# Kernel optimization log

Hardware: AMD Instinct MI355X
Metric: run time of the kernel (lower is better)

The kernel has to match this reference:

```python
import jax, jax.numpy as jnp
import numpy as np

BETA = 1.0
GAMMA = 0.25


def setup_inputs() -> dict:
    key = jax.random.key(0)
    ks = jax.random.split(key, 8)
    N, D_in, D_h, D_z = 65536, 1024, 512, 256
    s = lambda fan_in: 1.0 / np.sqrt(fan_in)
    return {
        "x": jax.random.normal(ks[0], (N, D_in), jnp.float32),
        "eW1": jax.random.normal(ks[1], (D_in, D_h), jnp.float32) * s(D_in),
        "eb1": jnp.zeros((D_h,), jnp.float32),
        "eW2": jax.random.normal(ks[2], (D_h, D_z), jnp.float32) * s(D_h),
        "eb2": jnp.zeros((D_z,), jnp.float32),
        "dW1": jax.random.normal(ks[3], (D_z, D_h), jnp.float32) * s(D_z),
        "db1": jnp.zeros((D_h,), jnp.float32),
        "dW2": jax.random.normal(ks[4], (D_h, D_in), jnp.float32) * s(D_h),
        "db2": jnp.zeros((D_in,), jnp.float32),
        "C0": jax.random.normal(ks[5], (1024, D_z), jnp.float32),
        "C1": jax.random.normal(ks[6], (512, D_z), jnp.float32),
        "C2": jax.random.normal(ks[7], (256, D_z), jnp.float32),
    }


def _nearest_idx(r, C):
    # argmin of squared euclidean distance == argmin of cdist(p=2)
    r = jax.lax.stop_gradient(r)
    d2 = jnp.sum(r * r, -1, keepdims=True) - 2.0 * (r @ C.T) + jnp.sum(C * C, -1)
    return jnp.argmin(d2, axis=-1)


def reference(x, eW1, eb1, eW2, eb2, dW1, db1, dW2, db2, C0, C1, C2):
    sg = jax.lax.stop_gradient
    # encoder: Linear -> GELU (exact) -> Linear
    z = jax.nn.gelu(x @ eW1 + eb1, approximate=False) @ eW2 + eb2
    residual = z
    output = jnp.zeros_like(z)
    losses = []
    for C in (C0, C1, C2):
        idx = _nearest_idx(residual, sg(C))
        q = C[idx]                                    # [N, 256] gather
        z2c = jnp.mean((residual - sg(q)) ** 2)       # commit input to code
        c2z = jnp.mean((sg(residual) - q) ** 2)       # move code to input
        losses.append(BETA * c2z + GAMMA * z2c)
        output = output + q
        residual = residual - q
    # straight-through: z + sg(zq) - sg(z)
    h = z + sg(output) - sg(z)
    out = jax.nn.gelu(h @ dW1 + db1, approximate=False) @ dW2 + db2
    recon_loss = jnp.mean((out - x) ** 2)
    return jnp.stack([recon_loss] + losses)  # [4]: recon, commit0, commit1, commit2
```

## Files before the change

### kernel.cpp

```cpp
#include <hip/hip_runtime.h>
#include <cstddef>


typedef __attribute__((ext_vector_type(8))) __bf16 bf16x8;
typedef __attribute__((ext_vector_type(4))) float f32x4;
typedef unsigned short u16;

__device__ __forceinline__ u16 f2bf(float f) {
    unsigned u = __float_as_uint(f);
    u += 0x7fffu + ((u >> 16) & 1u);
    return (u16)(u >> 16);
}
__device__ __forceinline__ float bf2f(u16 b) {
    return __uint_as_float((unsigned)b << 16);
}
__device__ __forceinline__ float gelu_exact(float v) {
    return 0.5f * v * (1.0f + erff(v * 0.7071067811865475f));
}
__device__ __forceinline__ void gload16(const void* g, void* l) {
    __builtin_amdgcn_global_load_lds(
        (const __attribute__((address_space(1))) void*)g,
        (__attribute__((address_space(3))) void*)l, 16, 0, 0);
}
__device__ __forceinline__ f32x4 mfma_bf16(bf16x8 a, bf16x8 b, f32x4 c) {
    return __builtin_amdgcn_mfma_f32_16x16x32_bf16(a, b, c, 0, 0, 0);
}

__global__ __launch_bounds__(256)
void prep_x(const float* __restrict__ x, u16* __restrict__ xbf)
{
    const size_t total = (size_t)65536 * 1024;
    const size_t step  = (size_t)gridDim.x * 256 * 8;
    for (size_t i = ((size_t)blockIdx.x * 256 + threadIdx.x) * 8; i < total; i += step) {
        float4 v0 = *(const float4*)&x[i];
        float4 v1 = *(const float4*)&x[i + 4];
        uint4 o;
        o.x = (unsigned)f2bf(v0.x) | ((unsigned)f2bf(v0.y) << 16);
        o.y = (unsigned)f2bf(v0.z) | ((unsigned)f2bf(v0.w) << 16);
        o.z = (unsigned)f2bf(v1.x) | ((unsigned)f2bf(v1.y) << 16);
        o.w = (unsigned)f2bf(v1.z) | ((unsigned)f2bf(v1.w) << 16);
        *(uint4*)&xbf[i] = o;
    }
}

__global__ __launch_bounds__(256)
void prep_weights(const float* __restrict__ eW1, const float* __restrict__ eW2,
                  const float* __restrict__ dW1, const float* __restrict__ dW2,
                  u16* __restrict__ eW1t, u16* __restrict__ eW2t,
                  u16* __restrict__ dW1t, u16* __restrict__ dW2t)
{
    const int b = blockIdx.x, t = threadIdx.x;
    if (b < 2048) {
        int e = b * 256 + t;
        int n = e >> 10, k = e & 1023;
        eW1t[e] = f2bf(eW1[(size_t)k * 512 + n]);
    } else if (b < 2560) {
        int e = (b - 2048) * 256 + t;
        int n = e >> 9, k = e & 511;
        eW2t[e] = f2bf(eW2[(size_t)k * 256 + n]);
    } else if (b < 3072) {
        int e = (b - 2560) * 256 + t;
        int n = e >> 8, k = e & 255;
        dW1t[e] = f2bf(dW1[(size_t)k * 512 + n]);
    } else {
        int e = (b - 3072) * 256 + t;
        int n = e >> 9, k = e & 511;
        dW2t[e] = f2bf(dW2[(size_t)k * 1024 + n]);
    }
}

__global__ __launch_bounds__(256)
void cb_prep(const float* __restrict__ C0, const float* __restrict__ C1,
             const float* __restrict__ C2, u16* __restrict__ Cbf,
             float* __restrict__ cnorm)
{
    __shared__ float red[256];
    const int code = blockIdx.x, t = threadIdx.x;
    const float* C;
    int local;
    if (code < 1024)      { C = C0; local = code; }
    else if (code < 1536) { C = C1; local = code - 1024; }
    else                  { C = C2; local = code - 1536; }
    const float v = C[(size_t)local * 256 + t];
    Cbf[(size_t)code * 256 + t] = f2bf(v);
    red[t] = v * v;
    __syncthreads();
    for (int s = 128; s; s >>= 1) { if (t < s) red[t] += red[t + s]; __syncthreads(); }
    if (t == 0) cnorm[code] = red[0];
}

template <int EPI>
__global__ __launch_bounds__(256, 2)
void gemm_mfma(const u16* __restrict__ A, const u16* __restrict__ Bt,
               const float* __restrict__ bias, u16* __restrict__ Obf,
               float* __restrict__ Of, const u16* __restrict__ Xbf,
               float* __restrict__ lossOut, int N, int K, int ntn,
               float lossScale)
{
    __shared__ __align__(16) u16 As[2][128 * 64];
    __shared__ __align__(16) u16 Bs[2][128 * 64];

    const int nwg = gridDim.x;
    const int bid = blockIdx.x;
    const int wg  = (bid & 7) * (nwg >> 3) + (bid >> 3);
    const int brow = (wg / ntn) * 128;
    const int bcol = (wg % ntn) * 128;

    const int t    = threadIdx.x;
    const int lane = t & 63;
    const int wid  = t >> 6;
    const int wrow = (wid >> 1) * 64, wcol = (wid & 1) * 64;
    const int lrow = lane & 15, g = lane >> 4;

    const int nt = K >> 6;

    f32x4 acc[4][4];
#pragma unroll
    for (int m = 0; m < 4; ++m)
#pragma unroll
        for (int n = 0; n < 4; ++n) acc[m][n] = (f32x4)0.f;

    auto stage = [&](const u16* __restrict__ src, int row0, int kt, u16* dst) {
#pragma unroll
        for (int it = 0; it < 4; ++it) {
            const int d   = (it * 256 + t) * 16;
            const int row = d >> 7;
            const int ch  = (d >> 4) & 7;
            const int cs  = ch ^ (row & 7);
            gload16(&src[(size_t)(row0 + row) * K + kt * 64 + cs * 8],
                    (char*)dst + d);
        }
    };

    stage(A, brow, 0, As[0]);
    stage(Bt, bcol, 0, Bs[0]);
    __syncthreads();

    int cur = 0;
    for (int kt = 0; kt < nt; ++kt) {
        if (kt + 1 < nt) {
            stage(A, brow, kt + 1, As[cur ^ 1]);
            stage(Bt, bcol, kt + 1, Bs[cur ^ 1]);
        }
#pragma unroll
        for (int ks = 0; ks < 2; ++ks) {
            bf16x8 a[4], b[4];
#pragma unroll
            for (int m = 0; m < 4; ++m) {
                const int R = wrow + m * 16 + lrow;
                a[m] = *(const bf16x8*)((const char*)&As[cur][0]
                         + R * 128 + (((ks * 4 + g) ^ (R & 7)) << 4));
            }
#pragma unroll
            for (int n = 0; n < 4; ++n) {
                const int R = wcol + n * 16 + lrow;
                b[n] = *(const bf16x8*)((const char*)&Bs[cur][0]
                         + R * 128 + (((ks * 4 + g) ^ (R & 7)) << 4));
            }
#pragma unroll
            for (int m = 0; m < 4; ++m)
#pragma unroll
                for (int n = 0; n < 4; ++n)
                    acc[m][n] = mfma_bf16(a[m], b[n], acc[m][n]);
        }
        __syncthreads();
        cur ^= 1;
    }

    int   colN[4];
    float bn[4];
#pragma unroll
    for (int n = 0; n < 4; ++n) {
        colN[n] = bcol + wcol + n * 16 + lrow;
        bn[n]   = bias[colN[n]];
    }

    if (EPI == 0) {
#pragma unroll
        for (int m = 0; m < 4; ++m) {
            const int rowb = brow + wrow + m * 16 + (lane >> 4) * 4;
#pragma unroll
            for (int n = 0; n < 4; ++n)
#pragma unroll
                for (int j = 0; j < 4; ++j)
                    Obf[(size_t)(rowb + j) * N + colN[n]] =
                        f2bf(gelu_exact(acc[m][n][j] + bn[n]));
        }
    } else if (EPI == 1) {
#pragma unroll
        for (int m = 0; m < 4; ++m) {
            const int rowb = brow + wrow + m * 16 + (lane >> 4) * 4;
#pragma unroll
            for (int n = 0; n < 4; ++n)
#pragma unroll
                for (int j = 0; j < 4; ++j)
                    Of[(size_t)(rowb + j) * N + colN[n]] = acc[m][n][j] + bn[n];
        }
    } else {
        float partial = 0.f;
#pragma unroll
        for (int m = 0; m < 4; ++m) {
            const int rowb = brow + wrow + m * 16 + (lane >> 4) * 4;
#pragma unroll
            for (int n = 0; n < 4; ++n)
#pragma unroll
                for (int j = 0; j < 4; ++j) {
                    const float o = acc[m][n][j] + bn[n];
                    const float d = o - bf2f(Xbf[(size_t)(rowb + j) * N + colN[n]]);
                    partial = fmaf(d, d, partial);
                }
        }
        float* red = (float*)&As[0][0];
        red[t] = partial;
        __syncthreads();
        for (int s = 128; s; s >>= 1) { if (t < s) red[t] += red[t + s]; __syncthreads(); }
        if (t == 0) atomicAdd(lossOut, red[0] * lossScale);
    }
}

__global__ __launch_bounds__(512, 4)
void vq_mfma(const float* __restrict__ Z, const u16* __restrict__ Cbf,
             const float* __restrict__ cnorm,
             const float* __restrict__ C0, const float* __restrict__ C1,
             const float* __restrict__ C2,
             u16* __restrict__ ZQ, float* __restrict__ lossOut)
{
    __shared__ __align__(16) u16 Rb[64][264];
    __shared__ __align__(16) u16 Cs[2][32 * 256];
    __shared__ float redv[64][2];
    __shared__ int   redi[64][2];
    __shared__ int   idxs[3][64];
    __shared__ float lred[8];

    const int t    = threadIdx.x;
    const int lane = t & 63;
    const int wid  = t >> 6;
    const int rg   = wid & 3;
    const int cg   = wid >> 2;
    const int lrow = lane & 15, g = lane >> 4;
    const int col  = t & 255;
    const int rh   = t >> 8;
    const int brow = blockIdx.x * 64;

    float R[32];
#pragma unroll
    for (int r = 0; r < 32; ++r)
        R[r] = Z[(size_t)(brow + rh * 32 + r) * 256 + col];

    const float* Cf[3]  = {C0, C1, C2};
    const int ncodes[3] = {1024, 512, 256};
    const int coff[3]   = {0, 1024, 1536};
    const float lscale  = 1.25f / (65536.0f * 256.0f);

    for (int stage = 0; stage < 3; ++stage) {
        const u16*   Cb  = Cbf + (size_t)coff[stage] * 256;
        const float* cns = cnorm + coff[stage];
        const int ntile  = ncodes[stage] >> 5;

        auto stageC = [&](int tile, int buf) {
#pragma unroll
            for (int it = 0; it < 2; ++it) {
                const int d   = (it * 512 + t) * 16;
                const int row = d >> 9;
                const int kb  = d & 511;
                const int kbs = kb ^ ((row & 7) << 4);
                gload16(&Cb[(size_t)(tile * 32 + row) * 256 + (kbs >> 1)],
                        (char*)&Cs[buf][0] + d);
            }
        };

        stageC(0, 0);
#pragma unroll
        for (int r = 0; r < 32; ++r) Rb[rh * 32 + r][col] = f2bf(R[r]);
        __syncthreads();

        bf16x8 a[8];
#pragma unroll
        for (int ks = 0; ks < 8; ++ks)
            a[ks] = *(const bf16x8*)&Rb[rg * 16 + lrow][ks * 32 + g * 8];

        float best[4]; int bidx[4];
#pragma unroll
        for (int j = 0; j < 4; ++j) { best[j] = 3.0e38f; bidx[j] = 0; }

        const int cr = cg * 16 + lrow;

        int buf = 0;
#pragma unroll 1
        for (int tile = 0; tile < ntile; ++tile) {
            if (tile + 1 < ntile) stageC(tile + 1, buf ^ 1);
            const int   code = tile * 32 + cr;
            const float cn   = cns[code];
            f32x4 acc = (f32x4)0.f;
#pragma unroll
            for (int ks = 0; ks < 8; ++ks) {
                const int kb = (ks * 64 + g * 16) ^ ((cr & 7) << 4);
                bf16x8 b = *(const bf16x8*)((const char*)&Cs[buf][0]
                             + cr * 512 + kb);
                acc = mfma_bf16(a[ks], b, acc);
            }
#pragma unroll
            for (int j = 0; j < 4; ++j) {
                const float s = fmaf(-2.0f, acc[j], cn);
                if (s < best[j]) { best[j] = s; bidx[j] = code; }
            }
            __syncthreads();
            buf ^= 1;
        }

#pragma unroll
        for (int j = 0; j < 4; ++j) {
            float v = best[j]; int i = bidx[j];
#pragma unroll
            for (int d = 1; d < 16; d <<= 1) {
                const float ov = __shfl_xor(v, d);
                const int   oi = __shfl_xor(i, d);
                if (ov < v || (ov == v && oi < i)) { v = ov; i = oi; }
            }
            if (lrow == 0) {
                redv[rg * 16 + g * 4 + j][cg] = v;
                redi[rg * 16 + g * 4 + j][cg] = i;
            }
        }
        __syncthreads();
        if (t < 64) {
            float v = redv[t][0]; int i = redi[t][0];
            const float ov = redv[t][1]; const int oi = redi[t][1];
            if (ov < v || (ov == v && oi < i)) { v = ov; i = oi; }
            idxs[stage][t] = i;
        }
        __syncthreads();

        const float* Cfs = Cf[stage];
        float partial = 0.f;
#pragma unroll
        for (int r = 0; r < 32; ++r) {
            const float q  = Cfs[(size_t)idxs[stage][rh * 32 + r] * 256 + col];
            const float rn = R[r] - q;
            R[r] = rn;
            partial = fmaf(rn, rn, partial);
        }
#pragma unroll
        for (int d = 32; d; d >>= 1) partial += __shfl_down(partial, d);
        if (lane == 0) lred[wid] = partial;
        __syncthreads();
        if (t == 0) {
            float s = 0.f;
#pragma unroll
            for (int w2 = 0; w2 < 8; ++w2) s += lred[w2];
            atomicAdd(&lossOut[1 + stage], s * lscale);
        }
        __syncthreads();
    }

#pragma unroll
    for (int r = 0; r < 32; ++r) {
        const int row = rh * 32 + r;
        const float zq = C0[(size_t)idxs[0][row] * 256 + col]
                       + C1[(size_t)idxs[1][row] * 256 + col]
                       + C2[(size_t)idxs[2][row] * 256 + col];
        ZQ[(size_t)(brow + row) * 256 + col] = f2bf(zq);
    }
}

extern "C" void kernel_launch(void* const* d_in, const int* in_sizes, int n_in,
                              void* d_out, int out_size, void* d_ws, size_t ws_size,
                              hipStream_t stream)
{
    const float* x   = (const float*)d_in[0];
    const float* eW1 = (const float*)d_in[1];
    const float* eb1 = (const float*)d_in[2];
    const float* eW2 = (const float*)d_in[3];
    const float* eb2 = (const float*)d_in[4];
    const float* dW1 = (const float*)d_in[5];
    const float* db1 = (const float*)d_in[6];
    const float* dW2 = (const float*)d_in[7];
    const float* db2 = (const float*)d_in[8];
    const float* C0  = (const float*)d_in[9];
    const float* C1  = (const float*)d_in[10];
    const float* C2  = (const float*)d_in[11];
    float* out = (float*)d_out;

    char* w = (char*)d_ws;
    u16*   H1   = (u16*)(w);
    float* Zf   = (float*)(w + ((size_t)64 << 20));
    u16*   ZQ   = (u16*)(w + ((size_t)128 << 20));
    u16*   H2   = (u16*)(w + ((size_t)160 << 20));
    u16*   xbf  = (u16*)(w + ((size_t)230 << 20));
    u16*   eW1t = (u16*)(w + ((size_t)224 << 20));
    u16*   eW2t = (u16*)(w + ((size_t)225 << 20));
    u16*   dW1t = (u16*)(w + ((size_t)226 << 20));
    u16*   dW2t = (u16*)(w + ((size_t)227 << 20));
    u16*   Cbf  = (u16*)(w + ((size_t)228 << 20));
    float* cn   = (float*)(w + ((size_t)229 << 20));

    hipMemsetAsync(d_out, 0, 4 * sizeof(float), stream);

    prep_x<<<4096, 256, 0, stream>>>(x, xbf);
    prep_weights<<<5120, 256, 0, stream>>>(eW1, eW2, dW1, dW2, eW1t, eW2t, dW1t, dW2t);
    cb_prep<<<1792, 256, 0, stream>>>(C0, C1, C2, Cbf, cn);

    gemm_mfma<0><<<2048, 256, 0, stream>>>(
        xbf, eW1t, eb1, H1, nullptr, nullptr, nullptr, 512, 1024, 4, 0.f);
    gemm_mfma<1><<<1024, 256, 0, stream>>>(
        H1, eW2t, eb2, nullptr, Zf, nullptr, nullptr, 256, 512, 2, 0.f);
    vq_mfma<<<1024, 512, 0, stream>>>(Zf, Cbf, cn, C0, C1, C2, ZQ, out);
    gemm_mfma<0><<<2048, 256, 0, stream>>>(
        ZQ, dW1t, db1, H2, nullptr, nullptr, nullptr, 512, 256, 4, 0.f);
    gemm_mfma<2><<<4096, 256, 0, stream>>>(
        H2, dW2t, db2, nullptr, nullptr, xbf, out, 1024, 512, 8,
        1.0f / (65536.0f * 1024.0f));
}
```

Baseline: 557.2 us.

## Use 256x128 GEMM tiles with 8 waves and triple-buffered LDS pipeline

The GEMM kernel now runs 512 threads per block on 256x128 output tiles, so each B tile is reused across more A rows. The LDS staging goes from double to triple buffering, with explicit vmcnt waits and a single raw barrier per k-step instead of two __syncthreads, so global loads run two tiles ahead of compute. It also raises wave priority around the MFMA section. LDS use grows to 144 KB per block, which may limit occupancy to one block per CU, and the launch grids are halved to match.

Result: slower. 599.6 us (+7.6%).

```diff
diff --git a/kernel.cpp b/kernel.cpp
--- a/kernel.cpp
+++ b/kernel.cpp
@@ -90,26 +90,27 @@
 }
 
 template <int EPI>
-__global__ __launch_bounds__(256, 2)
+__global__ __launch_bounds__(512, 2)
 void gemm_mfma(const u16* __restrict__ A, const u16* __restrict__ Bt,
                const float* __restrict__ bias, u16* __restrict__ Obf,
                float* __restrict__ Of, const u16* __restrict__ Xbf,
                float* __restrict__ lossOut, int N, int K, int ntn,
                float lossScale)
 {
-    __shared__ __align__(16) u16 As[2][128 * 64];
-    __shared__ __align__(16) u16 Bs[2][128 * 64];
+    __shared__ __align__(16) u16 As[3][256 * 64];
+    __shared__ __align__(16) u16 Bs[3][128 * 64];
 
     const int nwg = gridDim.x;
     const int bid = blockIdx.x;
     const int wg  = (bid & 7) * (nwg >> 3) + (bid >> 3);
-    const int brow = (wg / ntn) * 128;
+    const int brow = (wg / ntn) * 256;
     const int bcol = (wg % ntn) * 128;
 
     const int t    = threadIdx.x;
     const int lane = t & 63;
     const int wid  = t >> 6;
-    const int wrow = (wid >> 1) * 64, wcol = (wid & 1) * 64;
+    const int wrow = (wid & 3) * 64;
+    const int wcol = (wid >> 2) * 64;
     const int lrow = lane & 15, g = lane >> 4;
 
     const int nt = K >> 6;
@@ -120,42 +121,54 @@
 #pragma unroll
         for (int n = 0; n < 4; ++n) acc[m][n] = (f32x4)0.f;
 
-    auto stage = [&](const u16* __restrict__ src, int row0, int kt, u16* dst) {
+    auto stage = [&](int kt, int buf) {
 #pragma unroll
         for (int it = 0; it < 4; ++it) {
-            const int d   = (it * 256 + t) * 16;
+            const int d   = (it * 512 + t) * 16;
             const int row = d >> 7;
-            const int ch  = (d >> 4) & 7;
-            const int cs  = ch ^ (row & 7);
-            gload16(&src[(size_t)(row0 + row) * K + kt * 64 + cs * 8],
-                    (char*)dst + d);
+            const int cs  = ((d >> 4) & 7) ^ (row & 7);
+            gload16(&A[(size_t)(brow + row) * K + kt * 64 + cs * 8],
+                    (char*)&As[buf][0] + d);
+        }
+#pragma unroll
+        for (int it = 0; it < 2; ++it) {
+            const int d   = (it * 512 + t) * 16;
+            const int row = d >> 7;
+            const int cs  = ((d >> 4) & 7) ^ (row & 7);
+            gload16(&Bt[(size_t)(bcol + row) * K + kt * 64 + cs * 8],
+                    (char*)&Bs[buf][0] + d);
         }
     };
 
-    stage(A, brow, 0, As[0]);
-    stage(Bt, bcol, 0, Bs[0]);
-    __syncthreads();
-
-    int cur = 0;
+    stage(0, 0);
+    stage(1, 1);
+
     for (int kt = 0; kt < nt; ++kt) {
-        if (kt + 1 < nt) {
-            stage(A, brow, kt + 1, As[cur ^ 1]);
-            stage(Bt, bcol, kt + 1, Bs[cur ^ 1]);
-        }
+        if (kt < nt - 1) {
+            asm volatile("s_waitcnt vmcnt(6)" ::: "memory");
+        } else {
+            asm volatile("s_waitcnt vmcnt(0)" ::: "memory");
+        }
+        __builtin_amdgcn_s_barrier();
+        if (kt + 2 < nt) stage(kt + 2, (kt + 2) % 3);
+
+        const int buf = kt % 3;
+        const char* Ab = (const char*)&As[buf][0];
+        const char* Bb = (const char*)&Bs[buf][0];
+
+        __builtin_amdgcn_s_setprio(1);
 #pragma unroll
         for (int ks = 0; ks < 2; ++ks) {
             bf16x8 a[4], b[4];
 #pragma unroll
             for (int m = 0; m < 4; ++m) {
                 const int R = wrow + m * 16 + lrow;
-                a[m] = *(const bf16x8*)((const char*)&As[cur][0]
-                         + R * 128 + (((ks * 4 + g) ^ (R & 7)) << 4));
+                a[m] = *(const bf16x8*)(Ab + R * 128 + (((ks * 4 + g) ^ (R & 7)) << 4));
             }
 #pragma unroll
             for (int n = 0; n < 4; ++n) {
                 const int R = wcol + n * 16 + lrow;
-                b[n] = *(const bf16x8*)((const char*)&Bs[cur][0]
-                         + R * 128 + (((ks * 4 + g) ^ (R & 7)) << 4));
+                b[n] = *(const bf16x8*)(Bb + R * 128 + (((ks * 4 + g) ^ (R & 7)) << 4));
             }
 #pragma unroll
             for (int m = 0; m < 4; ++m)
@@ -163,8 +176,7 @@
                 for (int n = 0; n < 4; ++n)
                     acc[m][n] = mfma_bf16(a[m], b[n], acc[m][n]);
         }
-        __syncthreads();
-        cur ^= 1;
+        __builtin_amdgcn_s_setprio(0);
     }
 
     int   colN[4];
@@ -210,10 +222,11 @@
                     partial = fmaf(d, d, partial);
                 }
         }
+        __syncthreads();
         float* red = (float*)&As[0][0];
         red[t] = partial;
         __syncthreads();
-        for (int s = 128; s; s >>= 1) { if (t < s) red[t] += red[t + s]; __syncthreads(); }
+        for (int s = 256; s; s >>= 1) { if (t < s) red[t] += red[t + s]; __syncthreads(); }
         if (t == 0) atomicAdd(lossOut, red[0] * lossScale);
     }
 }
@@ -400,14 +413,14 @@
     prep_weights<<<5120, 256, 0, stream>>>(eW1, eW2, dW1, dW2, eW1t, eW2t, dW1t, dW2t);
     cb_prep<<<1792, 256, 0, stream>>>(C0, C1, C2, Cbf, cn);
 
-    gemm_mfma<0><<<2048, 256, 0, stream>>>(
+    gemm_mfma<0><<<1024, 512, 0, stream>>>(
         xbf, eW1t, eb1, H1, nullptr, nullptr, nullptr, 512, 1024, 4, 0.f);
-    gemm_mfma<1><<<1024, 256, 0, stream>>>(
+    gemm_mfma<1><<<512, 512, 0, stream>>>(
         H1, eW2t, eb2, nullptr, Zf, nullptr, nullptr, 256, 512, 2, 0.f);
     vq_mfma<<<1024, 512, 0, stream>>>(Zf, Cbf, cn, C0, C1, C2, ZQ, out);
-    gemm_mfma<0><<<2048, 256, 0, stream>>>(
+    gemm_mfma<0><<<1024, 512, 0, stream>>>(
         ZQ, dW1t, db1, H2, nullptr, nullptr, nullptr, 512, 256, 4, 0.f);
-    gemm_mfma<2><<<4096, 256, 0, stream>>>(
+    gemm_mfma<2><<<2048, 512, 0, stream>>>(
         H2, dW2t, db2, nullptr, nullptr, xbf, out, 1024, 512, 8,
         1.0f / (65536.0f * 1024.0f));
 }
```

## Enlarge GEMM tiles to 256x256 with 8 waves and split-K half-stage pipelining

Applied to the files above, without the earlier changes.

The bf16 MFMA GEMM moves from a 128x128 tile with 4 waves to a 256x256 tile with 8 waves, each wave computing 128x64. K tiles are staged in 32-wide halves, with a deeper prefetch scheme driven by explicit vmcnt waits and barriers, and MFMA bursts run at raised priority. The aim is more operand reuse per LDS load and better overlap of global loads with compute. The cost is fewer workgroups (256 to 1024), higher register pressure from 128 accumulator floats per lane, and more LDS per block, which may limit occupancy.

Result: faster. 541.3 us (-2.9%).

```diff
diff --git a/kernel.cpp b/kernel.cpp
--- a/kernel.cpp
+++ b/kernel.cpp
@@ -90,82 +90,108 @@
 }
 
 template <int EPI>
-__global__ __launch_bounds__(256, 2)
+__global__ __launch_bounds__(512, 2)
 void gemm_mfma(const u16* __restrict__ A, const u16* __restrict__ Bt,
                const float* __restrict__ bias, u16* __restrict__ Obf,
                float* __restrict__ Of, const u16* __restrict__ Xbf,
                float* __restrict__ lossOut, int N, int K, int ntn,
                float lossScale)
 {
-    __shared__ __align__(16) u16 As[2][128 * 64];
-    __shared__ __align__(16) u16 Bs[2][128 * 64];
+    __shared__ __align__(16) u16 SA[2][2][8192];
+    __shared__ __align__(16) u16 SB[2][2][8192];
 
     const int nwg = gridDim.x;
     const int bid = blockIdx.x;
     const int wg  = (bid & 7) * (nwg >> 3) + (bid >> 3);
-    const int brow = (wg / ntn) * 128;
-    const int bcol = (wg % ntn) * 128;
+    const int brow = (wg / ntn) * 256;
+    const int bcol = (wg % ntn) * 256;
 
     const int t    = threadIdx.x;
     const int lane = t & 63;
     const int wid  = t >> 6;
-    const int wrow = (wid >> 1) * 64, wcol = (wid & 1) * 64;
+    const int wrow = (wid >> 2) * 128;
+    const int wcol = (wid & 3) * 64;
     const int lrow = lane & 15, g = lane >> 4;
 
     const int nt = K >> 6;
 
-    f32x4 acc[4][4];
-#pragma unroll
-    for (int m = 0; m < 4; ++m)
+    f32x4 acc[8][4];
+#pragma unroll
+    for (int m = 0; m < 8; ++m)
 #pragma unroll
         for (int n = 0; n < 4; ++n) acc[m][n] = (f32x4)0.f;
 
-    auto stage = [&](const u16* __restrict__ src, int row0, int kt, u16* dst) {
-#pragma unroll
-        for (int it = 0; it < 4; ++it) {
-            const int d   = (it * 256 + t) * 16;
-            const int row = d >> 7;
-            const int ch  = (d >> 4) & 7;
-            const int cs  = ch ^ (row & 7);
-            gload16(&src[(size_t)(row0 + row) * K + kt * 64 + cs * 8],
-                    (char*)dst + d);
+    auto stage_half = [&](const u16* __restrict__ src, int row0, int Ts,
+                          int kh, char* region) {
+#pragma unroll
+        for (int it = 0; it < 2; ++it) {
+            const int d  = (it * 512 + t) * 16;
+            const int R  = d >> 6;
+            const int cs = ((d >> 4) & 3) ^ ((R >> 1) & 3);
+            gload16(&src[(size_t)(row0 + R) * K + Ts * 64 + kh * 32 + cs * 8],
+                    region + d);
         }
     };
 
-    stage(A, brow, 0, As[0]);
-    stage(Bt, bcol, 0, Bs[0]);
-    __syncthreads();
-
-    int cur = 0;
-    for (int kt = 0; kt < nt; ++kt) {
-        if (kt + 1 < nt) {
-            stage(A, brow, kt + 1, As[cur ^ 1]);
-            stage(Bt, bcol, kt + 1, Bs[cur ^ 1]);
-        }
-#pragma unroll
-        for (int ks = 0; ks < 2; ++ks) {
-            bf16x8 a[4], b[4];
-#pragma unroll
-            for (int m = 0; m < 4; ++m) {
-                const int R = wrow + m * 16 + lrow;
-                a[m] = *(const bf16x8*)((const char*)&As[cur][0]
-                         + R * 128 + (((ks * 4 + g) ^ (R & 7)) << 4));
-            }
-#pragma unroll
-            for (int n = 0; n < 4; ++n) {
-                const int R = wcol + n * 16 + lrow;
-                b[n] = *(const bf16x8*)((const char*)&Bs[cur][0]
-                         + R * 128 + (((ks * 4 + g) ^ (R & 7)) << 4));
-            }
-#pragma unroll
-            for (int m = 0; m < 4; ++m)
-#pragma unroll
-                for (int n = 0; n < 4; ++n)
-                    acc[m][n] = mfma_bf16(a[m], b[n], acc[m][n]);
-        }
-        __syncthreads();
-        cur ^= 1;
-    }
+    stage_half(A,  brow, 0, 0, (char*)&SA[0][0][0]);
+    stage_half(Bt, bcol, 0, 0, (char*)&SB[0][0][0]);
+    stage_half(A,  brow, 0, 1, (char*)&SA[0][1][0]);
+    stage_half(Bt, bcol, 0, 1, (char*)&SB[0][1][0]);
+    stage_half(A,  brow, 1, 0, (char*)&SA[1][0][0]);
+    stage_half(Bt, bcol, 1, 0, (char*)&SB[1][0][0]);
+    asm volatile("s_waitcnt vmcnt(8)" ::: "memory");
+    __builtin_amdgcn_s_barrier();
+
+    bf16x8 bfr[4];
+
+#define PHASE(MH, KK, DO_B, STAGE_CODE)                                        \
+    {                                                                          \
+        bf16x8 a_[4];                                                          \
+        _Pragma("unroll")                                                      \
+        for (int mi = 0; mi < 4; ++mi) {                                       \
+            const int R = wrow + ((MH) * 4 + mi) * 16 + lrow;                  \
+            a_[mi] = *(const bf16x8*)((const char*)&SA[d][KK][0]               \
+                      + R * 64 + ((g ^ ((R >> 1) & 3)) << 4));                 \
+        }                                                                      \
+        if (DO_B) {                                                            \
+            _Pragma("unroll")                                                  \
+            for (int n = 0; n < 4; ++n) {                                      \
+                const int R = wcol + n * 16 + lrow;                            \
+                bfr[n] = *(const bf16x8*)((const char*)&SB[d][KK][0]           \
+                          + R * 64 + ((g ^ ((R >> 1) & 3)) << 4));             \
+            }                                                                  \
+        }                                                                      \
+        STAGE_CODE;                                                            \
+        if (T >= nt - 2) asm volatile("s_waitcnt vmcnt(0)" ::: "memory");      \
+        else             asm volatile("s_waitcnt vmcnt(8)" ::: "memory");      \
+        __builtin_amdgcn_s_barrier();                                          \
+        __builtin_amdgcn_s_setprio(1);                                         \
+        _Pragma("unroll")                                                      \
+        for (int mi = 0; mi < 4; ++mi)                                         \
+            _Pragma("unroll")                                                  \
+            for (int n = 0; n < 4; ++n)                                        \
+                acc[(MH) * 4 + mi][n] =                                        \
+                    mfma_bf16(a_[mi], bfr[n], acc[(MH) * 4 + mi][n]);          \
+        __builtin_amdgcn_s_setprio(0);                                         \
+        __builtin_amdgcn_s_barrier();                                          \
+    }
+
+    for (int T = 0; T < nt; ++T) {
+        const int d = T & 1;
+        PHASE(0, 0, 1,
+              if (T + 1 < nt) stage_half(A, brow, T + 1, 1,
+                                         (char*)&SA[(T + 1) & 1][1][0]));
+        PHASE(1, 0, 0,
+              if (T + 1 < nt) stage_half(Bt, bcol, T + 1, 1,
+                                         (char*)&SB[(T + 1) & 1][1][0]));
+        PHASE(0, 1, 1,
+              if (T + 2 < nt) stage_half(A, brow, T + 2, 0,
+                                         (char*)&SA[T & 1][0][0]));
+        PHASE(1, 1, 0,
+              if (T + 2 < nt) stage_half(Bt, bcol, T + 2, 0,
+                                         (char*)&SB[T & 1][0][0]));
+    }
+#undef PHASE
 
     int   colN[4];
     float bn[4];
@@ -177,7 +203,7 @@
 
     if (EPI == 0) {
 #pragma unroll
-        for (int m = 0; m < 4; ++m) {
+        for (int m = 0; m < 8; ++m) {
             const int rowb = brow + wrow + m * 16 + (lane >> 4) * 4;
 #pragma unroll
             for (int n = 0; n < 4; ++n)
@@ -188,7 +214,7 @@
         }
     } else if (EPI == 1) {
 #pragma unroll
-        for (int m = 0; m < 4; ++m) {
+        for (int m = 0; m < 8; ++m) {
             const int rowb = brow + wrow + m * 16 + (lane >> 4) * 4;
 #pragma unroll
             for (int n = 0; n < 4; ++n)
@@ -199,7 +225,7 @@
     } else {
         float partial = 0.f;
 #pragma unroll
-        for (int m = 0; m < 4; ++m) {
+        for (int m = 0; m < 8; ++m) {
             const int rowb = brow + wrow + m * 16 + (lane >> 4) * 4;
 #pragma unroll
             for (int n = 0; n < 4; ++n)
@@ -210,10 +236,11 @@
                     partial = fmaf(d, d, partial);
                 }
         }
-        float* red = (float*)&As[0][0];
+        __syncthreads();
+        float* red = (float*)&SA[0][0][0];
         red[t] = partial;
         __syncthreads();
-        for (int s = 128; s; s >>= 1) { if (t < s) red[t] += red[t + s]; __syncthreads(); }
+        for (int s = 256; s; s >>= 1) { if (t < s) red[t] += red[t + s]; __syncthreads(); }
         if (t == 0) atomicAdd(lossOut, red[0] * lossScale);
     }
 }
@@ -400,14 +427,14 @@
     prep_weights<<<5120, 256, 0, stream>>>(eW1, eW2, dW1, dW2, eW1t, eW2t, dW1t, dW2t);
     cb_prep<<<1792, 256, 0, stream>>>(C0, C1, C2, Cbf, cn);
 
-    gemm_mfma<0><<<2048, 256, 0, stream>>>(
-        xbf, eW1t, eb1, H1, nullptr, nullptr, nullptr, 512, 1024, 4, 0.f);
-    gemm_mfma<1><<<1024, 256, 0, stream>>>(
-        H1, eW2t, eb2, nullptr, Zf, nullptr, nullptr, 256, 512, 2, 0.f);
+    gemm_mfma<0><<<512, 512, 0, stream>>>(
+        xbf, eW1t, eb1, H1, nullptr, nullptr, nullptr, 512, 1024, 2, 0.f);
+    gemm_mfma<1><<<256, 512, 0, stream>>>(
+        H1, eW2t, eb2, nullptr, Zf, nullptr, nullptr, 256, 512, 1, 0.f);
     vq_mfma<<<1024, 512, 0, stream>>>(Zf, Cbf, cn, C0, C1, C2, ZQ, out);
-    gemm_mfma<0><<<2048, 256, 0, stream>>>(
-        ZQ, dW1t, db1, H2, nullptr, nullptr, nullptr, 512, 256, 4, 0.f);
-    gemm_mfma<2><<<4096, 256, 0, stream>>>(
-        H2, dW2t, db2, nullptr, nullptr, xbf, out, 1024, 512, 8,
+    gemm_mfma<0><<<512, 512, 0, stream>>>(
+        ZQ, dW1t, db1, H2, nullptr, nullptr, nullptr, 512, 256, 2, 0.f);
+    gemm_mfma<2><<<1024, 512, 0, stream>>>(
+        H2, dW2t, db2, nullptr, nullptr, xbf, out, 1024, 512, 4,
         1.0f / (65536.0f * 1024.0f));
 }
```
